# Kernel optimization log

Measured on AMD Instinct MI355X. Metric: run time of the kernel, lower is better.

## Reference

```python
import jax, jax.numpy as jnp
import numpy as np

EPS = 1e-5
KH = KW = 3
PAD = 1

def conv3x3(x, w, b=None):
    out = jax.lax.conv_general_dilated(
        x, w, window_strides=(1, 1), padding=((PAD, PAD), (PAD, PAD)),
        dimension_numbers=("NCHW", "OIHW", "NCHW"))
    if b is not None:
        out = out + b[None, :, None, None]
    return out

def batchnorm(x, gamma, beta):
    # training-mode BatchNorm2d: batch statistics over (N, H, W)
    mean = x.mean(axis=(0, 2, 3), keepdims=True)
    var = x.var(axis=(0, 2, 3), keepdims=True)
    return gamma[None, :, None, None] * (x - mean) / jnp.sqrt(var + EPS) + beta[None, :, None, None]

def bilinear_gather(x, y_pos, x_pos):
    # x: [B,C,H,W]; y_pos/x_pos: [B,P,H,W] (P = KH*KW sampling taps)
    # zero padding outside image (mmcv modulated deform conv semantics)
    B, C, H, W = x.shape
    P = y_pos.shape[1]
    x_flat = x.reshape(B, C, H * W)
    y0 = jnp.floor(y_pos)
    x0 = jnp.floor(x_pos)
    ly = y_pos - y0
    lx = x_pos - x0
    out = jnp.zeros((B, C, P, H, W), dtype=x.dtype)
    for dy, dx, wgt in ((0, 0, (1 - ly) * (1 - lx)), (0, 1, (1 - ly) * lx),
                        (1, 0, ly * (1 - lx)), (1, 1, ly * lx)):
        yi = y0 + dy
        xi = x0 + dx
        valid = ((yi >= 0) & (yi <= H - 1) & (xi >= 0) & (xi <= W - 1)).astype(x.dtype)
        yc = jnp.clip(yi, 0, H - 1).astype(jnp.int32)
        xc = jnp.clip(xi, 0, W - 1).astype(jnp.int32)
        idx = (yc * W + xc).reshape(B, 1, P * H * W)
        vals = jnp.take_along_axis(x_flat, jnp.broadcast_to(idx, (B, C, P * H * W)), axis=2)
        vals = vals.reshape(B, C, P, H, W)
        out = out + vals * (wgt * valid)[:, None]
    return out  # [B,C,P,H,W]

def modulated_deform_conv(x, w_off, b_off, w_dcn):
    B, C, H, W = x.shape
    P = KH * KW
    off = conv3x3(x, w_off, b_off)  # [B, 3*P, H, W]
    o1, o2, m = jnp.split(off, 3, axis=1)
    offset = jnp.concatenate([o1, o2], axis=1)            # [B, 2P, H, W]
    offset = offset.reshape(B, P, 2, H, W)                # channel 2p -> dy, 2p+1 -> dx
    mask = jax.nn.sigmoid(m)                              # [B, P, H, W]
    hh = jnp.arange(H, dtype=x.dtype)
    ww = jnp.arange(W, dtype=x.dtype)
    ky = jnp.arange(KH, dtype=x.dtype)
    kx = jnp.arange(KW, dtype=x.dtype)
    # base sampling grid per tap p = ky*KW + kx: (h - PAD + ky, w - PAD + kx)
    base_y = (hh[None, :] - PAD + ky[:, None])            # [KH, H]
    base_x = (ww[None, :] - PAD + kx[:, None])            # [KW, W]
    base_y = jnp.broadcast_to(base_y[:, None, :, None], (KH, KW, H, W)).reshape(P, H, W)
    base_x = jnp.broadcast_to(base_x[None, :, None, :], (KH, KW, H, W)).reshape(P, H, W)
    y_pos = base_y[None] + offset[:, :, 0]                # [B,P,H,W]
    x_pos = base_x[None] + offset[:, :, 1]
    sampled = bilinear_gather(x, y_pos, x_pos)            # [B,C,P,H,W]
    sampled = sampled * mask[:, None]
    w = w_dcn.reshape(w_dcn.shape[0], C, P)               # [O, C, P]
    return jnp.einsum("bcphw,ocp->bohw", sampled, w)

def setup_inputs() -> dict:
    key = jax.random.key(0)
    ks = jax.random.split(key, 10)
    B, Ch, H, W = 4, 256, 64, 64
    Cin, Cout = 2 * Ch, 256
    P = KH * KW
    inp = {
        "input_v": jax.random.normal(ks[0], (B, Ch, H, W), jnp.float32),
        "input_i": jax.random.normal(ks[1], (B, Ch, H, W), jnp.float32),
        "w_off": jax.random.normal(ks[2], (3 * P, Cin, KH, KW), jnp.float32) * 0.01,
        "b_off": jnp.zeros((3 * P,), jnp.float32),
        "w_dcn": jax.random.normal(ks[3], (Cout, Cin, KH, KW), jnp.float32) * (1.0 / np.sqrt(Cin * P)),
        "gamma1": jnp.ones((Cout,), jnp.float32),
        "beta1": jnp.zeros((Cout,), jnp.float32),
        "w2": jax.random.normal(ks[4], (Cout, Cout, KH, KW), jnp.float32) * (1.0 / np.sqrt(Cout * P)),
        "gamma2": jnp.ones((Cout,), jnp.float32),
        "beta2": jnp.zeros((Cout,), jnp.float32),
    }
    return inp

def reference(input_v, input_i, w_off, b_off, w_dcn, gamma1, beta1, w2, gamma2, beta2):
    x = jnp.concatenate([input_v, input_i], axis=1)
    out = modulated_deform_conv(x, w_off, b_off, w_dcn)
    out = jax.nn.relu(batchnorm(out, gamma1, beta1))
    out = jax.nn.relu(batchnorm(conv3x3(out, w2), gamma2, beta2))
    return out
```

## Files before the change

kernel.cpp:

```cpp
#include <hip/hip_runtime.h>
#include <cstdint>
#include <cstddef>

typedef unsigned short u16;
typedef __attribute__((ext_vector_type(8))) short s16x8;
typedef __attribute__((ext_vector_type(4))) float f32x4;

#define DEV __device__ __forceinline__

DEV float bf2f(short u){
  union { unsigned int i; float f; } v;
  v.i = ((unsigned int)(u16)u) << 16;
  return v.f;
}
DEV short f2bf(float f){
  union { float f; unsigned int i; } v; v.f = f;
  unsigned int u = v.i;
  u += 0x7fffu + ((u >> 16) & 1u);
  return (short)(u >> 16);
}
DEV s16x8 s16x8_zero(){
  s16x8 z;
#pragma unroll
  for(int j=0;j<8;j++) z[j]=0;
  return z;
}
DEV f32x4 f32x4_zero(){
  f32x4 z;
#pragma unroll
  for(int j=0;j<4;j++) z[j]=0.f;
  return z;
}
DEV f32x4 mfma16(s16x8 a, s16x8 b, f32x4 c){
  return __builtin_amdgcn_mfma_f32_16x16x32_bf16(a, b, c, 0, 0, 0);
}
DEV void bar_lds(){
  asm volatile("s_waitcnt lgkmcnt(0)");
  __builtin_amdgcn_s_barrier();
}
DEV void gload16(const u16* g, u16* l){
  __builtin_amdgcn_global_load_lds(
      (const __attribute__((address_space(1))) unsigned int*)g,
      (__attribute__((address_space(3))) unsigned int*)l, 16, 0, 0);
}

static constexpr size_t OFF_ACC_B   = 0;
static constexpr size_t STATS_B     = 2097152;
static constexpr size_t OUT1_ACC_B  = 2101248;
static constexpr size_t OUT2_ACC_B  = 18878464;
static constexpr size_t XN_PAD_B    = 35655680;
static constexpr size_t OUT1N_PAD_B = 53497856;
static constexpr size_t ZERO_BYTES  = 62418944;
static constexpr size_t S_B         = 62418944;
static constexpr size_t WOFFT_B     = 213708800;
static constexpr size_t WDCNT_B     = 214003712;
static constexpr size_t W2T_B       = 216363008;
static constexpr size_t POFS_B      = 217542656;
static constexpr size_t PWGT_B      = 219901952;

__global__ void k_x_to_nhwc(const float* __restrict__ v, const float* __restrict__ vi,
                            u16* __restrict__ xn){
  __shared__ float tile[64][65];
  const int b = blockIdx.z, c0 = blockIdx.y*64, hw0 = blockIdx.x*64;
  const int h = hw0 >> 6;
  const float* src = (c0 < 256) ? (v  + ((size_t)b*256 + c0)      *4096)
                                : (vi + ((size_t)b*256 + (c0-256))*4096);
  const int t = threadIdx.x;
#pragma unroll
  for(int k=0;k<16;k++){
    int idx = t + k*256;
    int cl = idx >> 6, wl = idx & 63;
    tile[cl][wl] = src[(size_t)cl*4096 + hw0 + wl];
  }
  __syncthreads();
#pragma unroll
  for(int k=0;k<16;k++){
    int idx = t + k*256;
    int wl = idx >> 6, cl = idx & 63;
    xn[((size_t)(b*66 + h+1)*66 + wl+1)*512 + c0 + cl] = (u16)f2bf(tile[cl][wl]);
  }
}

__global__ void k_prep_woff(const float* __restrict__ w, u16* __restrict__ wt){
  int idx = blockIdx.x*256 + threadIdx.x;
  if(idx >= 32*4608) return;
  int n = idx / 4608, k = idx % 4608;
  int t = k >> 9, c = k & 511;
  float val = (n < 27) ? w[(size_t)(n*512 + c)*9 + t] : 0.f;
  wt[idx] = (u16)f2bf(val);
}
__global__ void k_prep_wdcn(const float* __restrict__ w, u16* __restrict__ wt){
  int idx = blockIdx.x*256 + threadIdx.x;
  if(idx >= 256*4608) return;
  int n = idx / 4608, k = idx % 4608;
  int t = k >> 9, c = k & 511;
  wt[idx] = (u16)f2bf(w[(size_t)(n*512 + c)*9 + t]);
}
__global__ void k_prep_w2(const float* __restrict__ w, u16* __restrict__ wt){
  int idx = blockIdx.x*256 + threadIdx.x;
  if(idx >= 256*2304) return;
  int n = idx / 2304, k = idx % 2304;
  int t = k >> 8, c = k & 255;
  wt[idx] = (u16)f2bf(w[(size_t)(n*256 + c)*9 + t]);
}

__global__ __launch_bounds__(256, 2) void k_conv_off(
    const u16* __restrict__ xn, const u16* __restrict__ wt, float* __restrict__ offa){
  __shared__ short A_lds[4][128][8];
  __shared__ short B_lds[4][32][8];
  const int tid = threadIdx.x;
  const int lane = tid & 63, wid = tid >> 6;
  const int quad = lane >> 4, ln = lane & 15;
  const int m0 = blockIdx.x * 128;
  const int b = m0 >> 12;
  const int h0 = (m0 & 4095) >> 6;
  const int ks = blockIdx.y;
  const int ts0 = (ks == 3) ? 6 : ks*2;
  const int ntap = (ks == 3) ? 3 : 2;
  const int m_base = wid * 32;
  const int r = tid >> 1, sp = (tid & 1) * 2;
  const int h_r = h0 + (r >> 6), w_r = r & 63;
  const s16x8* Ap = (const s16x8*)A_lds;
  const s16x8* Bp = (const s16x8*)B_lds;
  f32x4 acc[2][2];
#pragma unroll
  for(int mf=0;mf<2;mf++)
#pragma unroll
    for(int nf=0;nf<2;nf++) acc[mf][nf] = f32x4_zero();

  auto load_it = [&](int it, s16x8& v0, s16x8& v1, s16x8& bv){
    const int tp = ts0 + (it >> 4);
    const int cA = (it & 15)*32;
    const int ty = tp/3, tx = tp - ty*3;
    const int y = h_r + ty, x = w_r + tx;
    const u16* src = xn + ((size_t)(b*66 + y)*66 + x)*512 + cA + sp*8;
    v0 = *(const s16x8*)(src);
    v1 = *(const s16x8*)(src + 8);
    if(tid < 128){
      const int n = tid & 31, s2 = tid >> 5;
      bv = *(const s16x8*)(wt + (size_t)n*4608 + tp*512 + cA + s2*8);
    }
  };

  const int NIT = ntap * 16;
  s16x8 v0a, v1a, bva, v0b, v1b, bvb;
  bva = s16x8_zero(); bvb = s16x8_zero();
  load_it(0, v0a, v1a, bva);
  load_it(1, v0b, v1b, bvb);
  for(int it = 0; it < NIT; it += 2){
    bar_lds();
    *(s16x8*)(&A_lds[sp][r][0])   = v0a;
    *(s16x8*)(&A_lds[sp+1][r][0]) = v1a;
    if(tid < 128){
      const int n = tid & 31, s2 = tid >> 5;
      *(s16x8*)(&B_lds[s2][n][0]) = bva;
    }
    if(it + 2 < NIT) load_it(it + 2, v0a, v1a, bva);
    bar_lds();
    {
      s16x8 a0 = Ap[quad*128 + m_base + ln];
      s16x8 a1 = Ap[quad*128 + m_base + 16 + ln];
      s16x8 b0 = Bp[quad*32 + ln];
      s16x8 b1 = Bp[quad*32 + 16 + ln];
      acc[0][0] = mfma16(a0, b0, acc[0][0]);
      acc[0][1] = mfma16(a0, b1, acc[0][1]);
      acc[1][0] = mfma16(a1, b0, acc[1][0]);
      acc[1][1] = mfma16(a1, b1, acc[1][1]);
    }
    bar_lds();
    *(s16x8*)(&A_lds[sp][r][0])   = v0b;
    *(s16x8*)(&A_lds[sp+1][r][0]) = v1b;
    if(tid < 128){
      const int n = tid & 31, s2 = tid >> 5;
      *(s16x8*)(&B_lds[s2][n][0]) = bvb;
    }
    if(it + 3 < NIT) load_it(it + 3, v0b, v1b, bvb);
    bar_lds();
    {
      s16x8 a0 = Ap[quad*128 + m_base + ln];
      s16x8 a1 = Ap[quad*128 + m_base + 16 + ln];
      s16x8 b0 = Bp[quad*32 + ln];
      s16x8 b1 = Bp[quad*32 + 16 + ln];
      acc[0][0] = mfma16(a0, b0, acc[0][0]);
      acc[0][1] = mfma16(a0, b1, acc[0][1]);
      acc[1][0] = mfma16(a1, b0, acc[1][0]);
      acc[1][1] = mfma16(a1, b1, acc[1][1]);
    }
  }
#pragma unroll
  for(int mf=0;mf<2;mf++)
#pragma unroll
    for(int nf=0;nf<2;nf++){
      const int col = nf*16 + ln;
#pragma unroll
      for(int i=0;i<4;i++){
        const int row = m_base + mf*16 + quad*4 + i;
        unsafeAtomicAdd(offa + (size_t)(m0+row)*32 + col, acc[mf][nf][i]);
      }
    }
}

__global__ void k_prep_off2(const float* __restrict__ offa, const float* __restrict__ boff,
                            int* __restrict__ pofs, float* __restrict__ pwgt){
  int id = blockIdx.x*256 + threadIdx.x;
  if(id >= 16384*9) return;
  int m = id / 9, tp = id - m*9;
  int b = m >> 12, h = (m >> 6) & 63, w = m & 63;
  const float* orow = offa + (size_t)m*32;
  float dy = orow[2*tp]   + boff[2*tp];
  float dx = orow[2*tp+1] + boff[2*tp+1];
  float mz = orow[18+tp]  + boff[18+tp];
  float mk = 1.f / (1.f + expf(-mz));
  float ypos = (float)(h - 1 + tp/3) + dy;
  float xpos = (float)(w - 1 + tp%3) + dx;
  float y0f = floorf(ypos), x0f = floorf(xpos);
  float ly = ypos - y0f, lx = xpos - x0f;
  int y0 = (int)y0f, x0 = (int)x0f;
#pragma unroll
  for(int k=0;k<4;k++){
    int ddy = k >> 1, ddx = k & 1;
    int yi = y0 + ddy, xi = x0 + ddx;
    int yc = yi < -1 ? -1 : (yi > 64 ? 64 : yi);
    int xc = xi < -1 ? -1 : (xi > 64 ? 64 : xi);
    float wk = (ddy ? ly : 1.f-ly) * (ddx ? lx : 1.f-lx) * mk;
    pofs[id*4+k] = ((b*66 + yc+1)*66 + xc+1) << 9;
    pwgt[id*4+k] = wk;
  }
}

__global__ __launch_bounds__(256) void k_sample(
    const u16* __restrict__ xn, const int* __restrict__ pofs,
    const float* __restrict__ pwgt, u16* __restrict__ S){
  const int wid = threadIdx.x >> 6, lane = threadIdx.x & 63;
  const int m = blockIdx.x*4 + wid;
  const int tp = blockIdx.y;
  const int id4 = (m*9 + tp)*4;
  const int4   of = *(const int4*)  (pofs + id4);
  const float4 wg = *(const float4*)(pwgt + id4);
  const int c0 = lane*8;
  s16x8 g0 = *(const s16x8*)(xn + of.x + c0);
  s16x8 g1 = *(const s16x8*)(xn + of.y + c0);
  s16x8 g2 = *(const s16x8*)(xn + of.z + c0);
  s16x8 g3 = *(const s16x8*)(xn + of.w + c0);
  s16x8 pk;
#pragma unroll
  for(int j=0;j<8;j++){
    float f = wg.x * bf2f(g0[j]);
    f = fmaf(wg.y, bf2f(g1[j]), f);
    f = fmaf(wg.z, bf2f(g2[j]), f);
    f = fmaf(wg.w, bf2f(g3[j]), f);
    pk[j] = f2bf(f);
  }
  *(s16x8*)(S + (size_t)m*4608 + tp*512 + c0) = pk;
}

__global__ __launch_bounds__(256, 2) void k_gemm1(
    const u16* __restrict__ S, const u16* __restrict__ wt, float* __restrict__ outa){
  __shared__ short A_lds[2][8][128][8];
  __shared__ short B_lds[2][8][128][8];
  const int tid = threadIdx.x;
  const int lane = tid & 63, wid = tid >> 6;
  const int quad = lane >> 4, ln = lane & 15;
  const int wm = wid >> 1, wn = wid & 1;
  const int m0 = blockIdx.x * 128;
  const int n0 = blockIdx.y * 128;
  const int kbase = blockIdx.z * 2304;
  constexpr int NPH = 36;
  f32x4 acc[4][4];
#pragma unroll
  for(int mf=0;mf<4;mf++)
#pragma unroll
    for(int nf=0;nf<4;nf++) acc[mf][nf] = f32x4_zero();

  auto stage = [&](int t, int bi){
    const int k0 = kbase + t*64;
#pragma unroll
    for(int i=0;i<4;i++){
      const int idx = wid*4 + i;
      const int s = idx >> 1, rh = (idx & 1)*64;
      gload16(S  + (size_t)(m0 + rh + lane)*4608 + k0 + s*8, (u16*)&A_lds[bi][s][rh][0]);
      gload16(wt + (size_t)(n0 + rh + lane)*4608 + k0 + s*8, (u16*)&B_lds[bi][s][rh][0]);
    }
  };
  auto compute = [&](int bi){
#pragma unroll
    for(int kk=0;kk<2;kk++){
      s16x8 af[4], bf[4];
#pragma unroll
      for(int mf=0;mf<4;mf++)
        af[mf] = *(const s16x8*)&A_lds[bi][kk*4+quad][wm*64 + mf*16 + ln][0];
#pragma unroll
      for(int nf=0;nf<4;nf++)
        bf[nf] = *(const s16x8*)&B_lds[bi][kk*4+quad][wn*64 + nf*16 + ln][0];
#pragma unroll
      for(int mf=0;mf<4;mf++)
#pragma unroll
        for(int nf=0;nf<4;nf++)
          acc[mf][nf] = mfma16(af[mf], bf[nf], acc[mf][nf]);
    }
  };

  stage(0, 0);
  asm volatile("s_waitcnt vmcnt(0)");
  __builtin_amdgcn_s_barrier();
  stage(1, 1);
  for(int t = 0; t < NPH; ++t){
    const int bi = t & 1;
    compute(bi);
    bar_lds();
    if(t + 2 < NPH){
      stage(t + 2, bi);
      asm volatile("s_waitcnt vmcnt(8)");
    } else {
      asm volatile("s_waitcnt vmcnt(0)");
    }
    __builtin_amdgcn_sched_barrier(0);
    __builtin_amdgcn_s_barrier();
  }

#pragma unroll
  for(int mf=0;mf<4;mf++)
#pragma unroll
    for(int nf=0;nf<4;nf++){
      const int col = n0 + wn*64 + nf*16 + ln;
#pragma unroll
      for(int i=0;i<4;i++){
        const int row = m0 + wm*64 + mf*16 + quad*4 + i;
        unsafeAtomicAdd(outa + (size_t)row*256 + col, acc[mf][nf][i]);
      }
    }
}

__global__ __launch_bounds__(256, 2) void k_gemm2(
    const u16* __restrict__ a_pad, const u16* __restrict__ wt, float* __restrict__ outa){
  __shared__ short A_lds[2][8][128][8];
  __shared__ short B_lds[2][8][128][8];
  const int tid = threadIdx.x;
  const int lane = tid & 63, wid = tid >> 6;
  const int quad = lane >> 4, ln = lane & 15;
  const int wm = wid >> 1, wn = wid & 1;
  const int m0 = blockIdx.x * 128;
  const int n0 = blockIdx.y * 128;
  const int kbase = blockIdx.z * 1152;
  const int b = m0 >> 12;
  const int h0 = (m0 & 4095) >> 6;
  constexpr int NPH = 18;
  f32x4 acc[4][4];
#pragma unroll
  for(int mf=0;mf<4;mf++)
#pragma unroll
    for(int nf=0;nf<4;nf++) acc[mf][nf] = f32x4_zero();

  auto stage = [&](int t, int bi){
    const int k0 = kbase + t*64;
    const int tp = k0 >> 8, cit = k0 & 255;
    const int ty = tp/3, tx = tp - ty*3;
#pragma unroll
    for(int i=0;i<4;i++){
      const int idx = wid*4 + i;
      const int s = idx >> 1, rh = (idx & 1)*64;
      const int hh = h0 + (rh >> 6) + ty;
      gload16(a_pad + ((size_t)(b*66 + hh)*66 + lane + tx)*256 + cit + s*8,
              (u16*)&A_lds[bi][s][rh][0]);
      gload16(wt + (size_t)(n0 + rh + lane)*2304 + k0 + s*8,
              (u16*)&B_lds[bi][s][rh][0]);
    }
  };
  auto compute = [&](int bi){
#pragma unroll
    for(int kk=0;kk<2;kk++){
      s16x8 af[4], bf[4];
#pragma unroll
      for(int mf=0;mf<4;mf++)
        af[mf] = *(const s16x8*)&A_lds[bi][kk*4+quad][wm*64 + mf*16 + ln][0];
#pragma unroll
      for(int nf=0;nf<4;nf++)
        bf[nf] = *(const s16x8*)&B_lds[bi][kk*4+quad][wn*64 + nf*16 + ln][0];
#pragma unroll
      for(int mf=0;mf<4;mf++)
#pragma unroll
        for(int nf=0;nf<4;nf++)
          acc[mf][nf] = mfma16(af[mf], bf[nf], acc[mf][nf]);
    }
  };

  stage(0, 0);
  asm volatile("s_waitcnt vmcnt(0)");
  __builtin_amdgcn_s_barrier();
  stage(1, 1);
  for(int t = 0; t < NPH; ++t){
    const int bi = t & 1;
    compute(bi);
    bar_lds();
    if(t + 2 < NPH){
      stage(t + 2, bi);
      asm volatile("s_waitcnt vmcnt(8)");
    } else {
      asm volatile("s_waitcnt vmcnt(0)");
    }
    __builtin_amdgcn_sched_barrier(0);
    __builtin_amdgcn_s_barrier();
  }

#pragma unroll
  for(int mf=0;mf<4;mf++)
#pragma unroll
    for(int nf=0;nf<4;nf++){
      const int col = n0 + wn*64 + nf*16 + ln;
#pragma unroll
      for(int i=0;i<4;i++){
        const int row = m0 + wm*64 + mf*16 + quad*4 + i;
        unsafeAtomicAdd(outa + (size_t)row*256 + col, acc[mf][nf][i]);
      }
    }
}

__global__ void k_stats(const float* __restrict__ acc, float* __restrict__ sum,
                        float* __restrict__ sq){
  const int m0 = blockIdx.x*64;
  const int c = threadIdx.x;
  float s = 0.f, q = 0.f;
  for(int i=0;i<64;i++){
    float v = acc[(size_t)(m0+i)*256 + c];
    s += v; q += v*v;
  }
  unsafeAtomicAdd(sum + c, s);
  unsafeAtomicAdd(sq + c, q);
}

__global__ void k_bn1(const float* __restrict__ acc, const float* __restrict__ sum,
                      const float* __restrict__ sq, const float* __restrict__ g,
                      const float* __restrict__ bt, u16* __restrict__ o){
  __shared__ float sc[256], sh[256];
  const int t = threadIdx.x;
  {
    float mean = sum[t] * (1.f/16384.f);
    float var  = sq[t] * (1.f/16384.f) - mean*mean;
    float rstd = rsqrtf(var + 1e-5f);
    float s = g[t] * rstd;
    sc[t] = s; sh[t] = bt[t] - mean*s;
  }
  __syncthreads();
  const int c4 = (t & 63) * 4;
  const float s0 = sc[c4], s1 = sc[c4+1], s2 = sc[c4+2], s3 = sc[c4+3];
  const float h0 = sh[c4], h1 = sh[c4+1], h2 = sh[c4+2], h3 = sh[c4+3];
#pragma unroll
  for(int k=0;k<4;k++){
    int m = blockIdx.x*16 + k*4 + (t>>6);
    int b = m >> 12, hh = (m >> 6) & 63, ww = m & 63;
    const float4 v = *(const float4*)(acc + (size_t)m*256 + c4);
    unsigned int lo = (unsigned int)(u16)f2bf(fmaxf(0.f, v.x*s0 + h0))
                    | ((unsigned int)(u16)f2bf(fmaxf(0.f, v.y*s1 + h1)) << 16);
    unsigned int hi = (unsigned int)(u16)f2bf(fmaxf(0.f, v.z*s2 + h2))
                    | ((unsigned int)(u16)f2bf(fmaxf(0.f, v.w*s3 + h3)) << 16);
    uint2 pr; pr.x = lo; pr.y = hi;
    *(uint2*)(o + ((size_t)(b*66 + hh+1)*66 + ww+1)*256 + c4) = pr;
  }
}

__global__ void k_bn2_out(const float* __restrict__ acc, const float* __restrict__ sum,
                          const float* __restrict__ sq, const float* __restrict__ g,
                          const float* __restrict__ bt, float* __restrict__ out){
  __shared__ float tile[64][65];
  __shared__ float sc[64], sh[64];
  const int t = threadIdx.x;
  const int b = blockIdx.z, c0 = blockIdx.y*64, hw0 = blockIdx.x*64;
  if(t < 64){
    int c = c0 + t;
    float mean = sum[c] * (1.f/16384.f);
    float var  = sq[c] * (1.f/16384.f) - mean*mean;
    float rstd = rsqrtf(var + 1e-5f);
    float s = g[c] * rstd;
    sc[t] = s; sh[t] = bt[c] - mean*s;
  }
  __syncthreads();
#pragma unroll
  for(int k=0;k<16;k++){
    int idx = t + k*256;
    int wl = idx >> 6, cl = idx & 63;
    float v = acc[(size_t)((b<<12) + hw0 + wl)*256 + c0 + cl];
    tile[wl][cl] = fmaxf(0.f, v*sc[cl] + sh[cl]);
  }
  __syncthreads();
#pragma unroll
  for(int k=0;k<16;k++){
    int idx = t + k*256;
    int cl = idx >> 6, wl = idx & 63;
    out[(size_t)(b*256 + c0 + cl)*4096 + hw0 + wl] = tile[wl][cl];
  }
}

extern "C" void kernel_launch(void* const* d_in, const int* in_sizes, int n_in,
                              void* d_out, int out_size, void* d_ws, size_t ws_size,
                              hipStream_t stream){
  const float* in_v  = (const float*)d_in[0];
  const float* in_i  = (const float*)d_in[1];
  const float* w_off = (const float*)d_in[2];
  const float* b_off = (const float*)d_in[3];
  const float* w_dcn = (const float*)d_in[4];
  const float* g1    = (const float*)d_in[5];
  const float* bt1   = (const float*)d_in[6];
  const float* w2    = (const float*)d_in[7];
  const float* g2    = (const float*)d_in[8];
  const float* bt2   = (const float*)d_in[9];
  float* out = (float*)d_out;
  char* ws = (char*)d_ws;

  float* off_acc   = (float*)(ws + OFF_ACC_B);
  float* stats     = (float*)(ws + STATS_B);
  float* out1_acc  = (float*)(ws + OUT1_ACC_B);
  float* out2_acc  = (float*)(ws + OUT2_ACC_B);
  u16*   xn_pad    = (u16*)  (ws + XN_PAD_B);
  u16*   out1n_pad = (u16*)  (ws + OUT1N_PAD_B);
  u16*   Smat      = (u16*)  (ws + S_B);
  u16*   wofft     = (u16*)  (ws + WOFFT_B);
  u16*   wdcnt     = (u16*)  (ws + WDCNT_B);
  u16*   w2t       = (u16*)  (ws + W2T_B);
  int*   pofs      = (int*)  (ws + POFS_B);
  float* pwgt      = (float*)(ws + PWGT_B);
  float* sum1 = stats,       *sq1 = stats + 256;
  float* sum2 = stats + 512, *sq2 = stats + 768;

  hipMemsetAsync(ws, 0, ZERO_BYTES, stream);
  k_x_to_nhwc<<<dim3(64,8,4), 256, 0, stream>>>(in_v, in_i, xn_pad);
  k_prep_woff<<<576, 256, 0, stream>>>(w_off, wofft);
  k_prep_wdcn<<<4608, 256, 0, stream>>>(w_dcn, wdcnt);
  k_prep_w2<<<2304, 256, 0, stream>>>(w2, w2t);
  k_conv_off<<<dim3(128,4), 256, 0, stream>>>(xn_pad, wofft, off_acc);
  k_prep_off2<<<576, 256, 0, stream>>>(off_acc, b_off, pofs, pwgt);
  k_sample<<<dim3(4096,9), 256, 0, stream>>>(xn_pad, pofs, pwgt, Smat);
  k_gemm1<<<dim3(128,2,2), 256, 0, stream>>>(Smat, wdcnt, out1_acc);
  k_stats<<<256, 256, 0, stream>>>(out1_acc, sum1, sq1);
  k_bn1<<<1024, 256, 0, stream>>>(out1_acc, sum1, sq1, g1, bt1, out1n_pad);
  k_gemm2<<<dim3(128,2,2), 256, 0, stream>>>(out1n_pad, w2t, out2_acc);
  k_stats<<<256, 256, 0, stream>>>(out2_acc, sum2, sq2);
  k_bn2_out<<<dim3(64,4,4), 256, 0, stream>>>(out2_acc, sum2, sq2, g2, bt2, out);
}
```

Measured before the change: 392.5 us.

## Fuse bilinear sampling into DCN GEMM with producer-consumer warp specialization

```diff
diff --git a/kernel.cpp b/kernel.cpp
--- a/kernel.cpp
+++ b/kernel.cpp
@@ -35,7 +35,7 @@
   return __builtin_amdgcn_mfma_f32_16x16x32_bf16(a, b, c, 0, 0, 0);
 }
 DEV void bar_lds(){
-  asm volatile("s_waitcnt lgkmcnt(0)");
+  asm volatile("s_waitcnt lgkmcnt(0)" ::: "memory");
   __builtin_amdgcn_s_barrier();
 }
 DEV void gload16(const u16* g, u16* l){
@@ -51,7 +51,6 @@
 static constexpr size_t XN_PAD_B    = 35655680;
 static constexpr size_t OUT1N_PAD_B = 53497856;
 static constexpr size_t ZERO_BYTES  = 62418944;
-static constexpr size_t S_B         = 62418944;
 static constexpr size_t WOFFT_B     = 213708800;
 static constexpr size_t WDCNT_B     = 214003712;
 static constexpr size_t W2T_B       = 216363008;
@@ -228,107 +227,143 @@
   }
 }
 
-__global__ __launch_bounds__(256) void k_sample(
-    const u16* __restrict__ xn, const int* __restrict__ pofs,
-    const float* __restrict__ pwgt, u16* __restrict__ S){
-  const int wid = threadIdx.x >> 6, lane = threadIdx.x & 63;
-  const int m = blockIdx.x*4 + wid;
-  const int tp = blockIdx.y;
-  const int id4 = (m*9 + tp)*4;
-  const int4   of = *(const int4*)  (pofs + id4);
-  const float4 wg = *(const float4*)(pwgt + id4);
-  const int c0 = lane*8;
-  s16x8 g0 = *(const s16x8*)(xn + of.x + c0);
-  s16x8 g1 = *(const s16x8*)(xn + of.y + c0);
-  s16x8 g2 = *(const s16x8*)(xn + of.z + c0);
-  s16x8 g3 = *(const s16x8*)(xn + of.w + c0);
-  s16x8 pk;
-#pragma unroll
-  for(int j=0;j<8;j++){
-    float f = wg.x * bf2f(g0[j]);
-    f = fmaf(wg.y, bf2f(g1[j]), f);
-    f = fmaf(wg.z, bf2f(g2[j]), f);
-    f = fmaf(wg.w, bf2f(g3[j]), f);
-    pk[j] = f2bf(f);
-  }
-  *(s16x8*)(S + (size_t)m*4608 + tp*512 + c0) = pk;
-}
-
-__global__ __launch_bounds__(256, 2) void k_gemm1(
-    const u16* __restrict__ S, const u16* __restrict__ wt, float* __restrict__ outa){
-  __shared__ short A_lds[2][8][128][8];
-  __shared__ short B_lds[2][8][128][8];
+__global__ __launch_bounds__(512, 1) void k_dcn_pc(
+    const u16* __restrict__ xn, const u16* __restrict__ wt,
+    const int* __restrict__ pofs, const float* __restrict__ pwgt,
+    float* __restrict__ outa){
+  __shared__ short A_lds[2][8][64][8];
+  __shared__ short B_lds[2][8][256][8];
+  __shared__ int   s_ofs[9][4][64];
+  __shared__ float s_wgt[9][4][64];
   const int tid = threadIdx.x;
   const int lane = tid & 63, wid = tid >> 6;
   const int quad = lane >> 4, ln = lane & 15;
-  const int wm = wid >> 1, wn = wid & 1;
-  const int m0 = blockIdx.x * 128;
-  const int n0 = blockIdx.y * 128;
-  const int kbase = blockIdx.z * 2304;
-  constexpr int NPH = 36;
-  f32x4 acc[4][4];
-#pragma unroll
-  for(int mf=0;mf<4;mf++)
-#pragma unroll
-    for(int nf=0;nf<4;nf++) acc[mf][nf] = f32x4_zero();
-
-  auto stage = [&](int t, int bi){
-    const int k0 = kbase + t*64;
-#pragma unroll
-    for(int i=0;i<4;i++){
-      const int idx = wid*4 + i;
-      const int s = idx >> 1, rh = (idx & 1)*64;
-      gload16(S  + (size_t)(m0 + rh + lane)*4608 + k0 + s*8, (u16*)&A_lds[bi][s][rh][0]);
-      gload16(wt + (size_t)(n0 + rh + lane)*4608 + k0 + s*8, (u16*)&B_lds[bi][s][rh][0]);
-    }
-  };
-  auto compute = [&](int bi){
-#pragma unroll
-    for(int kk=0;kk<2;kk++){
-      s16x8 af[4], bf[4];
-#pragma unroll
-      for(int mf=0;mf<4;mf++)
-        af[mf] = *(const s16x8*)&A_lds[bi][kk*4+quad][wm*64 + mf*16 + ln][0];
-#pragma unroll
-      for(int nf=0;nf<4;nf++)
-        bf[nf] = *(const s16x8*)&B_lds[bi][kk*4+quad][wn*64 + nf*16 + ln][0];
-#pragma unroll
-      for(int mf=0;mf<4;mf++)
+  const int bid = blockIdx.x;
+  const int mb = (bid & 7)*32 + (bid >> 3);
+  const int m0 = mb * 64;
+  constexpr int NP = 72;
+
+  for(int i = tid; i < 576; i += 512){
+    const int rr = i & 63, tp = i >> 6;
+    const int id4 = ((m0 + rr)*9 + tp)*4;
+    int4   of = *(const int4*)  (pofs + id4);
+    float4 wg = *(const float4*)(pwgt + id4);
+    s_ofs[tp][0][rr] = of.x; s_ofs[tp][1][rr] = of.y;
+    s_ofs[tp][2][rr] = of.z; s_ofs[tp][3][rr] = of.w;
+    s_wgt[tp][0][rr] = wg.x; s_wgt[tp][1][rr] = wg.y;
+    s_wgt[tp][2][rr] = wg.z; s_wgt[tp][3][rr] = wg.w;
+  }
+  __syncthreads();
+
+  if(wid < 4){
+    const int wl = wid;
+    const int r  = wl*16 + (lane >> 2);
+    const int k8 = (lane & 3)*2;
+    s16x8 G[8];
+    s16x8 Bv[8];
+
+    auto bload = [&](int t){
+      const int tp = t >> 3, cc = (t & 7)*64;
+#pragma unroll
+      for(int i2=0;i2<8;i2++){
+        const int idx = wl*8 + i2;
+        const int s = idx >> 2, n0 = (idx & 3)*64;
+        Bv[i2] = *(const s16x8*)(wt + (size_t)(n0 + lane)*4608 + tp*512 + cc + s*8);
+      }
+    };
+    auto bwrite = [&](int bi){
+#pragma unroll
+      for(int i2=0;i2<8;i2++){
+        const int idx = wl*8 + i2;
+        const int s = idx >> 2, n0 = (idx & 3)*64;
+        *(s16x8*)&B_lds[bi][s][n0 + lane][0] = Bv[i2];
+      }
+    };
+    auto gatherG = [&](int t){
+      const int tp = t >> 3;
+      const int c0 = (t & 7)*64 + k8*8;
+#pragma unroll
+      for(int k=0;k<4;k++){
+        const u16* src = xn + s_ofs[tp][k][r] + c0;
+        G[k]   = *(const s16x8*)(src);
+        G[4+k] = *(const s16x8*)(src + 8);
+      }
+    };
+    auto blendW = [&](int t, int bi){
+      const int tp = t >> 3;
+      const float w0 = s_wgt[tp][0][r], w1 = s_wgt[tp][1][r];
+      const float w2 = s_wgt[tp][2][r], w3 = s_wgt[tp][3][r];
+      s16x8 p0, p1;
+#pragma unroll
+      for(int j=0;j<8;j++){
+        float f = w0*bf2f(G[0][j]); f = fmaf(w1, bf2f(G[1][j]), f);
+        f = fmaf(w2, bf2f(G[2][j]), f); f = fmaf(w3, bf2f(G[3][j]), f);
+        p0[j] = f2bf(f);
+        float g = w0*bf2f(G[4][j]); g = fmaf(w1, bf2f(G[5][j]), g);
+        g = fmaf(w2, bf2f(G[6][j]), g); g = fmaf(w3, bf2f(G[7][j]), g);
+        p1[j] = f2bf(g);
+      }
+      *(s16x8*)&A_lds[bi][k8][r][0]   = p0;
+      *(s16x8*)&A_lds[bi][k8+1][r][0] = p1;
+    };
+
+    bload(0); gatherG(0);
+    bwrite(0); blendW(0, 0);
+    bload(1); gatherG(1);
+    bar_lds();
+
+    for(int t = 0; t < NP; ++t){
+      const int nxt = (t + 1) & 1;
+      if(t + 1 < NP){
+        bwrite(nxt);
+        blendW(t + 1, nxt);
+      }
+      if(t + 2 < NP){
+        bload(t + 2);
+        gatherG(t + 2);
+      }
+      bar_lds();
+    }
+  } else {
+    const int wn = wid - 4;
+    f32x4 acc[4][4];
+#pragma unroll
+    for(int mf=0;mf<4;mf++)
+#pragma unroll
+      for(int nf=0;nf<4;nf++) acc[mf][nf] = f32x4_zero();
+
+    bar_lds();
+    for(int t = 0; t < NP; ++t){
+      const int bi = t & 1;
+#pragma unroll
+      for(int kk=0;kk<2;kk++){
+        s16x8 af[4], bf[4];
+#pragma unroll
+        for(int mf=0;mf<4;mf++)
+          af[mf] = *(const s16x8*)&A_lds[bi][kk*4+quad][mf*16 + ln][0];
 #pragma unroll
         for(int nf=0;nf<4;nf++)
-          acc[mf][nf] = mfma16(af[mf], bf[nf], acc[mf][nf]);
-    }
-  };
-
-  stage(0, 0);
-  asm volatile("s_waitcnt vmcnt(0)");
-  __builtin_amdgcn_s_barrier();
-  stage(1, 1);
-  for(int t = 0; t < NPH; ++t){
-    const int bi = t & 1;
-    compute(bi);
-    bar_lds();
-    if(t + 2 < NPH){
-      stage(t + 2, bi);
-      asm volatile("s_waitcnt vmcnt(8)");
-    } else {
-      asm volatile("s_waitcnt vmcnt(0)");
-    }
-    __builtin_amdgcn_sched_barrier(0);
-    __builtin_amdgcn_s_barrier();
-  }
-
-#pragma unroll
-  for(int mf=0;mf<4;mf++)
-#pragma unroll
-    for(int nf=0;nf<4;nf++){
-      const int col = n0 + wn*64 + nf*16 + ln;
-#pragma unroll
-      for(int i=0;i<4;i++){
-        const int row = m0 + wm*64 + mf*16 + quad*4 + i;
-        unsafeAtomicAdd(outa + (size_t)row*256 + col, acc[mf][nf][i]);
-      }
-    }
+          bf[nf] = *(const s16x8*)&B_lds[bi][kk*4+quad][wn*64 + nf*16 + ln][0];
+#pragma unroll
+        for(int mf=0;mf<4;mf++)
+#pragma unroll
+          for(int nf=0;nf<4;nf++)
+            acc[mf][nf] = mfma16(af[mf], bf[nf], acc[mf][nf]);
+      }
+      bar_lds();
+    }
+#pragma unroll
+    for(int mf=0;mf<4;mf++)
+#pragma unroll
+      for(int nf=0;nf<4;nf++){
+        const int col = wn*64 + nf*16 + ln;
+#pragma unroll
+        for(int i=0;i<4;i++){
+          const int row = m0 + mf*16 + quad*4 + i;
+          outa[(size_t)row*256 + col] = acc[mf][nf][i];
+        }
+      }
+  }
 }
 
 __global__ __launch_bounds__(256, 2) void k_gemm2(
@@ -385,7 +420,7 @@
   };
 
   stage(0, 0);
-  asm volatile("s_waitcnt vmcnt(0)");
+  asm volatile("s_waitcnt vmcnt(0)" ::: "memory");
   __builtin_amdgcn_s_barrier();
   stage(1, 1);
   for(int t = 0; t < NPH; ++t){
@@ -394,9 +429,9 @@
     bar_lds();
     if(t + 2 < NPH){
       stage(t + 2, bi);
-      asm volatile("s_waitcnt vmcnt(8)");
+      asm volatile("s_waitcnt vmcnt(8)" ::: "memory");
     } else {
-      asm volatile("s_waitcnt vmcnt(0)");
+      asm volatile("s_waitcnt vmcnt(0)" ::: "memory");
     }
     __builtin_amdgcn_sched_barrier(0);
     __builtin_amdgcn_s_barrier();
@@ -512,7 +547,6 @@
   float* out2_acc  = (float*)(ws + OUT2_ACC_B);
   u16*   xn_pad    = (u16*)  (ws + XN_PAD_B);
   u16*   out1n_pad = (u16*)  (ws + OUT1N_PAD_B);
-  u16*   Smat      = (u16*)  (ws + S_B);
   u16*   wofft     = (u16*)  (ws + WOFFT_B);
   u16*   wdcnt     = (u16*)  (ws + WDCNT_B);
   u16*   w2t       = (u16*)  (ws + W2T_B);
@@ -528,8 +562,7 @@
   k_prep_w2<<<2304, 256, 0, stream>>>(w2, w2t);
   k_conv_off<<<dim3(128,4), 256, 0, stream>>>(xn_pad, wofft, off_acc);
   k_prep_off2<<<576, 256, 0, stream>>>(off_acc, b_off, pofs, pwgt);
-  k_sample<<<dim3(4096,9), 256, 0, stream>>>(xn_pad, pofs, pwgt, Smat);
-  k_gemm1<<<dim3(128,2,2), 256, 0, stream>>>(Smat, wdcnt, out1_acc);
+  k_dcn_pc<<<256, 512, 0, stream>>>(xn_pad, wdcnt, pofs, pwgt, out1_acc);
   k_stats<<<256, 256, 0, stream>>>(out1_acc, sum1, sq1);
   k_bn1<<<1024, 256, 0, stream>>>(out1_acc, sum1, sq1, g1, bt1, out1n_pad);
   k_gemm2<<<dim3(128,2,2), 256, 0, stream>>>(out1n_pad, w2t, out2_acc);
```

Result: faster. 376.4 us (-4.1%).

## Reorder deformable conv as per-pixel GEMM then bilinear combine of projected features

Applied to the files above, without the earlier changes.

```diff
diff --git a/kernel.cpp b/kernel.cpp
--- a/kernel.cpp
+++ b/kernel.cpp
@@ -19,12 +19,6 @@
   u += 0x7fffu + ((u >> 16) & 1u);
   return (short)(u >> 16);
 }
-DEV s16x8 s16x8_zero(){
-  s16x8 z;
-#pragma unroll
-  for(int j=0;j<8;j++) z[j]=0;
-  return z;
-}
 DEV f32x4 f32x4_zero(){
   f32x4 z;
 #pragma unroll
@@ -35,7 +29,7 @@
   return __builtin_amdgcn_mfma_f32_16x16x32_bf16(a, b, c, 0, 0, 0);
 }
 DEV void bar_lds(){
-  asm volatile("s_waitcnt lgkmcnt(0)");
+  asm volatile("s_waitcnt lgkmcnt(0)" ::: "memory");
   __builtin_amdgcn_s_barrier();
 }
 DEV void gload16(const u16* g, u16* l){
@@ -44,19 +38,17 @@
       (__attribute__((address_space(3))) unsigned int*)l, 16, 0, 0);
 }
 
-static constexpr size_t OFF_ACC_B   = 0;
-static constexpr size_t STATS_B     = 2097152;
-static constexpr size_t OUT1_ACC_B  = 2101248;
-static constexpr size_t OUT2_ACC_B  = 18878464;
-static constexpr size_t XN_PAD_B    = 35655680;
-static constexpr size_t OUT1N_PAD_B = 53497856;
-static constexpr size_t ZERO_BYTES  = 62418944;
-static constexpr size_t S_B         = 62418944;
-static constexpr size_t WOFFT_B     = 213708800;
-static constexpr size_t WDCNT_B     = 214003712;
-static constexpr size_t W2T_B       = 216363008;
-static constexpr size_t POFS_B      = 217542656;
-static constexpr size_t PWGT_B      = 219901952;
+static constexpr size_t STATS_B     = 0;
+static constexpr size_t OUT2_ACC_B  = 4096;
+static constexpr size_t XN_PAD_B    = 16781312;
+static constexpr size_t OUT1N_PAD_B = 34738176;
+static constexpr size_t ZERO_BYTES  = 43659264;
+static constexpr size_t OUT1_ACC_B  = 43659264;
+static constexpr size_t PPIX_B      = 60436480;
+static constexpr size_t PWGT_B      = 62795776;
+static constexpr size_t Y_B         = 65155072;
+static constexpr size_t WALL_B      = 159428608;
+static constexpr size_t W2T_B       = 162181120;
 
 __global__ void k_x_to_nhwc(const float* __restrict__ v, const float* __restrict__ vi,
                             u16* __restrict__ xn){
@@ -81,20 +73,20 @@
   }
 }
 
-__global__ void k_prep_woff(const float* __restrict__ w, u16* __restrict__ wt){
+__global__ void k_prep_wall(const float* __restrict__ wdcn, const float* __restrict__ woff,
+                            u16* __restrict__ wt){
   int idx = blockIdx.x*256 + threadIdx.x;
-  if(idx >= 32*4608) return;
-  int n = idx / 4608, k = idx % 4608;
-  int t = k >> 9, c = k & 511;
-  float val = (n < 27) ? w[(size_t)(n*512 + c)*9 + t] : 0.f;
+  if(idx >= 2688*512) return;
+  int n = idx >> 9, c = idx & 511;
+  float val = 0.f;
+  if(n < 2304){
+    int p = n >> 8, o = n & 255;
+    val = wdcn[(size_t)(o*512 + c)*9 + p];
+  } else if(n < 2592){
+    int q = n - 2304, p = q >> 5, nn = q & 31;
+    if(nn < 27) val = woff[(size_t)(nn*512 + c)*9 + p];
+  }
   wt[idx] = (u16)f2bf(val);
-}
-__global__ void k_prep_wdcn(const float* __restrict__ w, u16* __restrict__ wt){
-  int idx = blockIdx.x*256 + threadIdx.x;
-  if(idx >= 256*4608) return;
-  int n = idx / 4608, k = idx % 4608;
-  int t = k >> 9, c = k & 511;
-  wt[idx] = (u16)f2bf(w[(size_t)(n*512 + c)*9 + t]);
 }
 __global__ void k_prep_w2(const float* __restrict__ w, u16* __restrict__ wt){
   int idx = blockIdx.x*256 + threadIdx.x;
@@ -104,158 +96,8 @@
   wt[idx] = (u16)f2bf(w[(size_t)(n*256 + c)*9 + t]);
 }
 
-__global__ __launch_bounds__(256, 2) void k_conv_off(
-    const u16* __restrict__ xn, const u16* __restrict__ wt, float* __restrict__ offa){
-  __shared__ short A_lds[4][128][8];
-  __shared__ short B_lds[4][32][8];
-  const int tid = threadIdx.x;
-  const int lane = tid & 63, wid = tid >> 6;
-  const int quad = lane >> 4, ln = lane & 15;
-  const int m0 = blockIdx.x * 128;
-  const int b = m0 >> 12;
-  const int h0 = (m0 & 4095) >> 6;
-  const int ks = blockIdx.y;
-  const int ts0 = (ks == 3) ? 6 : ks*2;
-  const int ntap = (ks == 3) ? 3 : 2;
-  const int m_base = wid * 32;
-  const int r = tid >> 1, sp = (tid & 1) * 2;
-  const int h_r = h0 + (r >> 6), w_r = r & 63;
-  const s16x8* Ap = (const s16x8*)A_lds;
-  const s16x8* Bp = (const s16x8*)B_lds;
-  f32x4 acc[2][2];
-#pragma unroll
-  for(int mf=0;mf<2;mf++)
-#pragma unroll
-    for(int nf=0;nf<2;nf++) acc[mf][nf] = f32x4_zero();
-
-  auto load_it = [&](int it, s16x8& v0, s16x8& v1, s16x8& bv){
-    const int tp = ts0 + (it >> 4);
-    const int cA = (it & 15)*32;
-    const int ty = tp/3, tx = tp - ty*3;
-    const int y = h_r + ty, x = w_r + tx;
-    const u16* src = xn + ((size_t)(b*66 + y)*66 + x)*512 + cA + sp*8;
-    v0 = *(const s16x8*)(src);
-    v1 = *(const s16x8*)(src + 8);
-    if(tid < 128){
-      const int n = tid & 31, s2 = tid >> 5;
-      bv = *(const s16x8*)(wt + (size_t)n*4608 + tp*512 + cA + s2*8);
-    }
-  };
-
-  const int NIT = ntap * 16;
-  s16x8 v0a, v1a, bva, v0b, v1b, bvb;
-  bva = s16x8_zero(); bvb = s16x8_zero();
-  load_it(0, v0a, v1a, bva);
-  load_it(1, v0b, v1b, bvb);
-  for(int it = 0; it < NIT; it += 2){
-    bar_lds();
-    *(s16x8*)(&A_lds[sp][r][0])   = v0a;
-    *(s16x8*)(&A_lds[sp+1][r][0]) = v1a;
-    if(tid < 128){
-      const int n = tid & 31, s2 = tid >> 5;
-      *(s16x8*)(&B_lds[s2][n][0]) = bva;
-    }
-    if(it + 2 < NIT) load_it(it + 2, v0a, v1a, bva);
-    bar_lds();
-    {
-      s16x8 a0 = Ap[quad*128 + m_base + ln];
-      s16x8 a1 = Ap[quad*128 + m_base + 16 + ln];
-      s16x8 b0 = Bp[quad*32 + ln];
-      s16x8 b1 = Bp[quad*32 + 16 + ln];
-      acc[0][0] = mfma16(a0, b0, acc[0][0]);
-      acc[0][1] = mfma16(a0, b1, acc[0][1]);
-      acc[1][0] = mfma16(a1, b0, acc[1][0]);
-      acc[1][1] = mfma16(a1, b1, acc[1][1]);
-    }
-    bar_lds();
-    *(s16x8*)(&A_lds[sp][r][0])   = v0b;
-    *(s16x8*)(&A_lds[sp+1][r][0]) = v1b;
-    if(tid < 128){
-      const int n = tid & 31, s2 = tid >> 5;
-      *(s16x8*)(&B_lds[s2][n][0]) = bvb;
-    }
-    if(it + 3 < NIT) load_it(it + 3, v0b, v1b, bvb);
-    bar_lds();
-    {
-      s16x8 a0 = Ap[quad*128 + m_base + ln];
-      s16x8 a1 = Ap[quad*128 + m_base + 16 + ln];
-      s16x8 b0 = Bp[quad*32 + ln];
-      s16x8 b1 = Bp[quad*32 + 16 + ln];
-      acc[0][0] = mfma16(a0, b0, acc[0][0]);
-      acc[0][1] = mfma16(a0, b1, acc[0][1]);
-      acc[1][0] = mfma16(a1, b0, acc[1][0]);
-      acc[1][1] = mfma16(a1, b1, acc[1][1]);
-    }
-  }
-#pragma unroll
-  for(int mf=0;mf<2;mf++)
-#pragma unroll
-    for(int nf=0;nf<2;nf++){
-      const int col = nf*16 + ln;
-#pragma unroll
-      for(int i=0;i<4;i++){
-        const int row = m_base + mf*16 + quad*4 + i;
-        unsafeAtomicAdd(offa + (size_t)(m0+row)*32 + col, acc[mf][nf][i]);
-      }
-    }
-}
-
-__global__ void k_prep_off2(const float* __restrict__ offa, const float* __restrict__ boff,
-                            int* __restrict__ pofs, float* __restrict__ pwgt){
-  int id = blockIdx.x*256 + threadIdx.x;
-  if(id >= 16384*9) return;
-  int m = id / 9, tp = id - m*9;
-  int b = m >> 12, h = (m >> 6) & 63, w = m & 63;
-  const float* orow = offa + (size_t)m*32;
-  float dy = orow[2*tp]   + boff[2*tp];
-  float dx = orow[2*tp+1] + boff[2*tp+1];
-  float mz = orow[18+tp]  + boff[18+tp];
-  float mk = 1.f / (1.f + expf(-mz));
-  float ypos = (float)(h - 1 + tp/3) + dy;
-  float xpos = (float)(w - 1 + tp%3) + dx;
-  float y0f = floorf(ypos), x0f = floorf(xpos);
-  float ly = ypos - y0f, lx = xpos - x0f;
-  int y0 = (int)y0f, x0 = (int)x0f;
-#pragma unroll
-  for(int k=0;k<4;k++){
-    int ddy = k >> 1, ddx = k & 1;
-    int yi = y0 + ddy, xi = x0 + ddx;
-    int yc = yi < -1 ? -1 : (yi > 64 ? 64 : yi);
-    int xc = xi < -1 ? -1 : (xi > 64 ? 64 : xi);
-    float wk = (ddy ? ly : 1.f-ly) * (ddx ? lx : 1.f-lx) * mk;
-    pofs[id*4+k] = ((b*66 + yc+1)*66 + xc+1) << 9;
-    pwgt[id*4+k] = wk;
-  }
-}
-
-__global__ __launch_bounds__(256) void k_sample(
-    const u16* __restrict__ xn, const int* __restrict__ pofs,
-    const float* __restrict__ pwgt, u16* __restrict__ S){
-  const int wid = threadIdx.x >> 6, lane = threadIdx.x & 63;
-  const int m = blockIdx.x*4 + wid;
-  const int tp = blockIdx.y;
-  const int id4 = (m*9 + tp)*4;
-  const int4   of = *(const int4*)  (pofs + id4);
-  const float4 wg = *(const float4*)(pwgt + id4);
-  const int c0 = lane*8;
-  s16x8 g0 = *(const s16x8*)(xn + of.x + c0);
-  s16x8 g1 = *(const s16x8*)(xn + of.y + c0);
-  s16x8 g2 = *(const s16x8*)(xn + of.z + c0);
-  s16x8 g3 = *(const s16x8*)(xn + of.w + c0);
-  s16x8 pk;
-#pragma unroll
-  for(int j=0;j<8;j++){
-    float f = wg.x * bf2f(g0[j]);
-    f = fmaf(wg.y, bf2f(g1[j]), f);
-    f = fmaf(wg.z, bf2f(g2[j]), f);
-    f = fmaf(wg.w, bf2f(g3[j]), f);
-    pk[j] = f2bf(f);
-  }
-  *(s16x8*)(S + (size_t)m*4608 + tp*512 + c0) = pk;
-}
-
-__global__ __launch_bounds__(256, 2) void k_gemm1(
-    const u16* __restrict__ S, const u16* __restrict__ wt, float* __restrict__ outa){
+__global__ __launch_bounds__(256, 2) void k_gemm_big(
+    const u16* __restrict__ A, const u16* __restrict__ wt, u16* __restrict__ Y){
   __shared__ short A_lds[2][8][128][8];
   __shared__ short B_lds[2][8][128][8];
   const int tid = threadIdx.x;
@@ -264,8 +106,7 @@
   const int wm = wid >> 1, wn = wid & 1;
   const int m0 = blockIdx.x * 128;
   const int n0 = blockIdx.y * 128;
-  const int kbase = blockIdx.z * 2304;
-  constexpr int NPH = 36;
+  constexpr int NPH = 8;
   f32x4 acc[4][4];
 #pragma unroll
   for(int mf=0;mf<4;mf++)
@@ -273,13 +114,13 @@
     for(int nf=0;nf<4;nf++) acc[mf][nf] = f32x4_zero();
 
   auto stage = [&](int t, int bi){
-    const int k0 = kbase + t*64;
+    const int k0 = t*64;
 #pragma unroll
     for(int i=0;i<4;i++){
       const int idx = wid*4 + i;
       const int s = idx >> 1, rh = (idx & 1)*64;
-      gload16(S  + (size_t)(m0 + rh + lane)*4608 + k0 + s*8, (u16*)&A_lds[bi][s][rh][0]);
-      gload16(wt + (size_t)(n0 + rh + lane)*4608 + k0 + s*8, (u16*)&B_lds[bi][s][rh][0]);
+      gload16(A  + (size_t)(m0 + rh + lane)*512 + k0 + s*8, (u16*)&A_lds[bi][s][rh][0]);
+      gload16(wt + (size_t)(n0 + rh + lane)*512 + k0 + s*8, (u16*)&B_lds[bi][s][rh][0]);
     }
   };
   auto compute = [&](int bi){
@@ -301,7 +142,7 @@
   };
 
   stage(0, 0);
-  asm volatile("s_waitcnt vmcnt(0)");
+  asm volatile("s_waitcnt vmcnt(0)" ::: "memory");
   __builtin_amdgcn_s_barrier();
   stage(1, 1);
   for(int t = 0; t < NPH; ++t){
@@ -310,9 +151,9 @@
     bar_lds();
     if(t + 2 < NPH){
       stage(t + 2, bi);
-      asm volatile("s_waitcnt vmcnt(8)");
+      asm volatile("s_waitcnt vmcnt(8)" ::: "memory");
     } else {
-      asm volatile("s_waitcnt vmcnt(0)");
+      asm volatile("s_waitcnt vmcnt(0)" ::: "memory");
     }
     __builtin_amdgcn_sched_barrier(0);
     __builtin_amdgcn_s_barrier();
@@ -326,9 +167,107 @@
 #pragma unroll
       for(int i=0;i<4;i++){
         const int row = m0 + wm*64 + mf*16 + quad*4 + i;
-        unsafeAtomicAdd(outa + (size_t)row*256 + col, acc[mf][nf][i]);
+        Y[(size_t)row*2688 + col] = (u16)f2bf(acc[mf][nf][i]);
       }
     }
+}
+
+__global__ __launch_bounds__(256) void k_off_combine(
+    const u16* __restrict__ Y, const float* __restrict__ boff,
+    int* __restrict__ ppix, float* __restrict__ pwgt){
+  __shared__ float offs[64][32];
+  const int t = threadIdx.x;
+  const int b = blockIdx.x >> 6, h = blockIdx.x & 63;
+  const int w = t >> 2, g = t & 3;
+  float acc[8];
+#pragma unroll
+  for(int j=0;j<8;j++) acc[j] = 0.f;
+  for(int p=0;p<9;p++){
+    const int pp = (b*66 + h + p/3)*66 + (w + p%3);
+    s16x8 v = *(const s16x8*)(Y + (size_t)pp*2688 + 2304 + p*32 + g*8);
+#pragma unroll
+    for(int j=0;j<8;j++) acc[j] += bf2f(v[j]);
+  }
+#pragma unroll
+  for(int j=0;j<8;j++) offs[w][g*8 + j] = acc[j];
+  __syncthreads();
+  for(int id = t; id < 576; id += 256){
+    const int tp = id / 64, ww = id & 63;
+    const int m = (b<<12) + (h<<6) + ww;
+    float dy = offs[ww][2*tp]   + boff[2*tp];
+    float dx = offs[ww][2*tp+1] + boff[2*tp+1];
+    float mz = offs[ww][18+tp]  + boff[18+tp];
+    float mk = 1.f / (1.f + expf(-mz));
+    float ypos = (float)(h - 1 + tp/3) + dy;
+    float xpos = (float)(ww - 1 + tp%3) + dx;
+    float y0f = floorf(ypos), x0f = floorf(xpos);
+    float ly = ypos - y0f, lx = xpos - x0f;
+    int y0 = (int)y0f, x0 = (int)x0f;
+    const int id4 = (m*9 + tp)*4;
+#pragma unroll
+    for(int k=0;k<4;k++){
+      int ddy = k >> 1, ddx = k & 1;
+      int yi = y0 + ddy, xi = x0 + ddx;
+      int yc = yi < -1 ? -1 : (yi > 64 ? 64 : yi);
+      int xc = xi < -1 ? -1 : (xi > 64 ? 64 : xi);
+      float wk = (ddy ? ly : 1.f-ly) * (ddx ? lx : 1.f-lx) * mk;
+      ppix[id4+k] = (b*66 + yc+1)*66 + xc+1;
+      pwgt[id4+k] = wk;
+    }
+  }
+}
+
+__global__ __launch_bounds__(512) void k_combine(
+    const u16* __restrict__ Y, const int* __restrict__ ppix,
+    const float* __restrict__ pwgt, float* __restrict__ out1){
+  __shared__ int   s_pp[64][9][4];
+  __shared__ float s_wg[64][9][4];
+  const int t = threadIdx.x;
+  const int b = blockIdx.x >> 6, h = blockIdx.x & 63;
+  const int m_row = (b<<12) + (h<<6);
+  for(int id = t; id < 576; id += 512){
+    const int mo = id / 9, tp = id - mo*9;
+    const size_t i4 = ((size_t)(m_row + mo)*9 + tp)*4;
+    int4   pp4 = *(const int4*)  (ppix + i4);
+    float4 wg4 = *(const float4*)(pwgt + i4);
+    s_pp[mo][tp][0] = pp4.x; s_pp[mo][tp][1] = pp4.y;
+    s_pp[mo][tp][2] = pp4.z; s_pp[mo][tp][3] = pp4.w;
+    s_wg[mo][tp][0] = wg4.x; s_wg[mo][tp][1] = wg4.y;
+    s_wg[mo][tp][2] = wg4.z; s_wg[mo][tp][3] = wg4.w;
+  }
+  __syncthreads();
+  const int wv = t >> 6, lane = t & 63;
+  const int c0 = lane*4;
+  const int pw0 = wv*8;
+  float acc[8][4];
+#pragma unroll
+  for(int pw=0;pw<8;pw++)
+#pragma unroll
+    for(int j=0;j<4;j++) acc[pw][j] = 0.f;
+
+  for(int tp = 0; tp < 9; ++tp){
+    const int cb = tp*256 + c0;
+#pragma unroll
+    for(int pw=0;pw<8;pw++){
+      const int px = pw0 + pw;
+#pragma unroll
+      for(int k=0;k<4;k++){
+        const float wk = s_wg[px][tp][k];
+        const int   pp = s_pp[px][tp][k];
+        ushort4 v = *(const ushort4*)(Y + (size_t)pp*2688 + cb);
+        acc[pw][0] = fmaf(wk, bf2f((short)v.x), acc[pw][0]);
+        acc[pw][1] = fmaf(wk, bf2f((short)v.y), acc[pw][1]);
+        acc[pw][2] = fmaf(wk, bf2f((short)v.z), acc[pw][2]);
+        acc[pw][3] = fmaf(wk, bf2f((short)v.w), acc[pw][3]);
+      }
+    }
+  }
+#pragma unroll
+  for(int pw=0;pw<8;pw++){
+    float4 o4;
+    o4.x = acc[pw][0]; o4.y = acc[pw][1]; o4.z = acc[pw][2]; o4.w = acc[pw][3];
+    *(float4*)(out1 + (size_t)(m_row + pw0 + pw)*256 + c0) = o4;
+  }
 }
 
 __global__ __launch_bounds__(256, 2) void k_gemm2(
@@ -385,7 +324,7 @@
   };
 
   stage(0, 0);
-  asm volatile("s_waitcnt vmcnt(0)");
+  asm volatile("s_waitcnt vmcnt(0)" ::: "memory");
   __builtin_amdgcn_s_barrier();
   stage(1, 1);
   for(int t = 0; t < NPH; ++t){
@@ -394,9 +333,9 @@
     bar_lds();
     if(t + 2 < NPH){
       stage(t + 2, bi);
-      asm volatile("s_waitcnt vmcnt(8)");
+      asm volatile("s_waitcnt vmcnt(8)" ::: "memory");
     } else {
-      asm volatile("s_waitcnt vmcnt(0)");
+      asm volatile("s_waitcnt vmcnt(0)" ::: "memory");
     }
     __builtin_amdgcn_sched_barrier(0);
     __builtin_amdgcn_s_barrier();
@@ -506,30 +445,26 @@
   float* out = (float*)d_out;
   char* ws = (char*)d_ws;
 
-  float* off_acc   = (float*)(ws + OFF_ACC_B);
   float* stats     = (float*)(ws + STATS_B);
-  float* out1_acc  = (float*)(ws + OUT1_ACC_B);
   float* out2_acc  = (float*)(ws + OUT2_ACC_B);
   u16*   xn_pad    = (u16*)  (ws + XN_PAD_B);
   u16*   out1n_pad = (u16*)  (ws + OUT1N_PAD_B);
-  u16*   Smat      = (u16*)  (ws + S_B);
-  u16*   wofft     = (u16*)  (ws + WOFFT_B);
-  u16*   wdcnt     = (u16*)  (ws + WDCNT_B);
+  float* out1_acc  = (float*)(ws + OUT1_ACC_B);
+  int*   ppix      = (int*)  (ws + PPIX_B);
+  float* pwgt      = (float*)(ws + PWGT_B);
+  u16*   Ymat      = (u16*)  (ws + Y_B);
+  u16*   wall      = (u16*)  (ws + WALL_B);
   u16*   w2t       = (u16*)  (ws + W2T_B);
-  int*   pofs      = (int*)  (ws + POFS_B);
-  float* pwgt      = (float*)(ws + PWGT_B);
   float* sum1 = stats,       *sq1 = stats + 256;
   float* sum2 = stats + 512, *sq2 = stats + 768;
 
   hipMemsetAsync(ws, 0, ZERO_BYTES, stream);
   k_x_to_nhwc<<<dim3(64,8,4), 256, 0, stream>>>(in_v, in_i, xn_pad);
-  k_prep_woff<<<576, 256, 0, stream>>>(w_off, wofft);
-  k_prep_wdcn<<<4608, 256, 0, stream>>>(w_dcn, wdcnt);
+  k_prep_wall<<<5376, 256, 0, stream>>>(w_dcn, w_off, wall);
   k_prep_w2<<<2304, 256, 0, stream>>>(w2, w2t);
-  k_conv_off<<<dim3(128,4), 256, 0, stream>>>(xn_pad, wofft, off_acc);
-  k_prep_off2<<<576, 256, 0, stream>>>(off_acc, b_off, pofs, pwgt);
-  k_sample<<<dim3(4096,9), 256, 0, stream>>>(xn_pad, pofs, pwgt, Smat);
-  k_gemm1<<<dim3(128,2,2), 256, 0, stream>>>(Smat, wdcnt, out1_acc);
+  k_gemm_big<<<dim3(137,21), 256, 0, stream>>>(xn_pad, wall, Ymat);
+  k_off_combine<<<256, 256, 0, stream>>>(Ymat, b_off, ppix, pwgt);
+  k_combine<<<256, 512, 0, stream>>>(Ymat, ppix, pwgt, out1_acc);
   k_stats<<<256, 256, 0, stream>>>(out1_acc, sum1, sq1);
   k_bn1<<<1024, 256, 0, stream>>>(out1_acc, sum1, sq1, g1, bt1, out1n_pad);
   k_gemm2<<<dim3(128,2,2), 256, 0, stream>>>(out1n_pad, w2t, out2_acc);
```

Result: faster. 370.4 us (-5.6%).
